# Optimization experiments

Measured on AMD Instinct MI355X. Metric: run time of the kernel, lower is better.

Reference implementation:

```python
import jax, jax.numpy as jnp
import numpy as np

DIM = 256
HEADS = 8
NX = NY = 48
RNG = 5
MAX_IDX = (RNG + 1) ** 2  # 36, padding token


def _make_tokens(nx, ny, rng):
    # Half-symmetric tokenization of 2D relative positions (Learnable_rel_pos_embedding.tokenize)
    xm, ym = np.meshgrid(np.arange(nx), np.arange(ny), indexing='ij')
    xm, ym = xm.ravel(), ym.ravel()
    dx = xm[None, :] - xm[:, None]
    dy = ym[None, :] - ym[:, None]
    tok = np.abs(dx) * (rng + 1) + np.abs(dy)
    tok[(np.abs(dx) > rng) | (np.abs(dy) > rng)] = MAX_IDX
    return tok.astype(np.int32)


def setup_inputs() -> dict:
    key = jax.random.key(0)
    ks = jax.random.split(key, 10)
    s = DIM ** -0.5
    x = jax.random.normal(ks[0], (1, DIM, NX, NY), dtype=jnp.float32)
    Wq = jax.random.normal(ks[1], (DIM, DIM), dtype=jnp.float32) * s
    bq = jax.random.normal(ks[2], (DIM,), dtype=jnp.float32) * 0.01
    Wk = jax.random.normal(ks[3], (DIM, DIM), dtype=jnp.float32) * s
    bk = jax.random.normal(ks[4], (DIM,), dtype=jnp.float32) * 0.01
    Wv = jax.random.normal(ks[5], (DIM, DIM), dtype=jnp.float32) * s
    bv = jax.random.normal(ks[6], (DIM,), dtype=jnp.float32) * 0.01
    Wp = jax.random.normal(ks[7], (DIM, DIM), dtype=jnp.float32) * s
    bp = jax.random.normal(ks[8], (DIM,), dtype=jnp.float32) * 0.01
    emb = jax.random.normal(ks[9], (MAX_IDX + 1, HEADS), dtype=jnp.float32) * 0.02
    tokens = jnp.asarray(_make_tokens(NX, NY, RNG))  # (N, N) int32
    return dict(x=x, Wq=Wq, bq=bq, Wk=Wk, bk=bk, Wv=Wv, bv=bv,
                Wp=Wp, bp=bp, emb=emb, tokens=tokens)


def reference(x, Wq, bq, Wk, bk, Wv, bv, Wp, bp, emb, tokens):
    B, C, nx, ny = x.shape
    H = emb.shape[1]
    hd = C // H
    N = nx * ny
    scale = hd ** -0.5

    def conv1x1(W, b, t):
        return (jnp.einsum('oc,bcxy->boxy', W, t) + b[None, :, None, None])

    # Q/K/V as 1x1 convs, split into heads: (B, H, hd, N)
    q = conv1x1(Wq, bq, x).reshape(B, H, hd, N)
    k = conv1x1(Wk, bk, x).reshape(B, H, hd, N)
    v = conv1x1(Wv, bv, x).reshape(B, H, hd, N)

    # attn_method=2: scores = scale*QK^T + relative positional bias
    scores = jnp.einsum('bhdn,bhdm->bhnm', q, k) * scale  # (B, H, N, N)

    # pos_type=5: embedding lookup over half-symmetric relative-position tokens
    pad = emb.shape[0] - 1
    emb_masked = emb.at[pad].set(0.0)  # padding_idx row is zero
    pe = emb_masked[tokens]            # (N, N, H)
    scores = scores + jnp.transpose(pe, (2, 0, 1))[None]

    attn = jax.nn.softmax(scores, axis=-1)
    out = jnp.einsum('bhnm,bhdm->bhdn', attn, v).reshape(B, C, nx, ny)
    out = conv1x1(Wp, bp, out)
    return out
```

## Files before the change

kernel.cpp:

```cpp
#include <hip/hip_runtime.h>

#define NN 2304
#define CC 256
#define HH 8
#define HD 32
#define NYY 48
#define SCALE 0.17677669529663687f

typedef __bf16 bf16_t;
typedef __bf16 bf8v __attribute__((ext_vector_type(8)));
typedef float f4v __attribute__((ext_vector_type(4)));

__device__ __forceinline__ f4v mfma16(bf8v a, bf8v b, f4v c) {
    return __builtin_amdgcn_mfma_f32_16x16x32_bf16(a, b, c, 0, 0, 0);
}

__global__ __launch_bounds__(256) void k_xT(const float* __restrict__ x,
                                            bf16_t* __restrict__ xT) {
    __shared__ float tile[64][33];
    const int c0 = (blockIdx.x & 7) * 32;
    const int n0 = (blockIdx.x >> 3) * 64;
    const int t = threadIdx.x;
    const int n = t & 63, cb = t >> 6;
#pragma unroll
    for (int cc = 0; cc < 8; cc++) {
        int c = cc * 4 + cb;
        tile[n][c] = x[(size_t)(c0 + c) * NN + n0 + n];
    }
    __syncthreads();
    const int c = t & 31, nb = t >> 5;
#pragma unroll
    for (int nn = 0; nn < 8; nn++) {
        int n2 = nn * 8 + nb;
        xT[(size_t)(n0 + n2) * CC + c0 + c] = (bf16_t)tile[n2][c];
    }
}

__global__ __launch_bounds__(256) void k_proj_qkv(
    const float* __restrict__ Wq, const float* __restrict__ bq,
    const float* __restrict__ Wk, const float* __restrict__ bk,
    const float* __restrict__ Wv, const float* __restrict__ bv,
    const bf16_t* __restrict__ xT,
    bf16_t* __restrict__ Qt, bf16_t* __restrict__ Kt, bf16_t* __restrict__ Vd) {
    const int mat = blockIdx.z;
    const float* W = (mat == 0) ? Wq : (mat == 1) ? Wk : Wv;
    const float* bias = (mat == 0) ? bq : (mat == 1) ? bk : bv;
    const int n0 = blockIdx.x * 64;
    const int o0 = blockIdx.y * 64;
    const int lane = threadIdx.x & 63;
    const int wave = threadIdx.x >> 6;
    const int l15 = lane & 15;
    const int quad = lane >> 4;
    const int orow = o0 + wave * 16;

    f4v acc[4];
#pragma unroll
    for (int i = 0; i < 4; i++) acc[i] = f4v{0.f, 0.f, 0.f, 0.f};

    for (int k0 = 0; k0 < CC; k0 += 32) {
        const float* wp = W + (size_t)(orow + l15) * CC + k0 + quad * 8;
        float4 wa = *(const float4*)wp;
        float4 wb = *(const float4*)(wp + 4);
        bf8v af;
        af[0] = (bf16_t)wa.x; af[1] = (bf16_t)wa.y;
        af[2] = (bf16_t)wa.z; af[3] = (bf16_t)wa.w;
        af[4] = (bf16_t)wb.x; af[5] = (bf16_t)wb.y;
        af[6] = (bf16_t)wb.z; af[7] = (bf16_t)wb.w;
#pragma unroll
        for (int nb = 0; nb < 4; nb++) {
            bf8v bfv = *(const bf8v*)(xT + (size_t)(n0 + nb * 16 + l15) * CC + k0 + quad * 8);
            acc[nb] = mfma16(af, bfv, acc[nb]);
        }
    }

#pragma unroll
    for (int r = 0; r < 4; r++) {
        const int o = orow + quad * 4 + r;
        const float bo = bias[o];
#pragma unroll
        for (int nb = 0; nb < 4; nb++) {
            const int n = n0 + nb * 16 + l15;
            float v = acc[nb][r] + bo;
            if (mat == 2) {
                Vd[(size_t)o * NN + n] = (bf16_t)v;
            } else {
                int h = o >> 5, d = o & 31;
                bf16_t* dst = (mat == 0) ? Qt : Kt;
                float vv = (mat == 0) ? v * SCALE : v;
                dst[(size_t)h * NN * HD + (size_t)n * HD + d] = (bf16_t)vv;
            }
        }
    }
}

__global__ __launch_bounds__(256) void k_attn(
    const bf16_t* __restrict__ Qt, const bf16_t* __restrict__ Kt,
    const bf16_t* __restrict__ Vd, const float* __restrict__ emb,
    bf16_t* __restrict__ Yt) {
    __shared__ float lds_emb[40];
    __shared__ bf16_t lds_p[4][16 * 32];
    const int h = blockIdx.x & 7;
    const int qt = blockIdx.x >> 3;
    const int t = threadIdx.x;
    if (t < 37) lds_emb[t] = (t < 36) ? emb[t * HH + h] : 0.0f;
    __syncthreads();

    const int wave = t >> 6, lane = t & 63;
    const int l15 = lane & 15, quad = lane >> 4;
    const int qg0 = qt * 64 + wave * 16;
    const bf16_t* Qh = Qt + (size_t)h * NN * HD;
    const bf16_t* Kh = Kt + (size_t)h * NN * HD;
    const bf16_t* Vh = Vd + (size_t)h * HD * NN;

    const bf8v aq = *(const bf8v*)(Qh + (size_t)(qg0 + l15) * HD + quad * 8);

    int xi[4], yi[4];
#pragma unroll
    for (int r = 0; r < 4; r++) {
        int qi = qg0 + quad * 4 + r;
        xi[r] = qi / NYY;
        yi[r] = qi - xi[r] * NYY;
    }

    f4v o0 = {0.f, 0.f, 0.f, 0.f}, o1 = {0.f, 0.f, 0.f, 0.f};
    const f4v z = {0.f, 0.f, 0.f, 0.f};
    float lsum[4] = {0.f, 0.f, 0.f, 0.f};
    bf16_t* pl = &lds_p[wave][0];

    for (int kb = 0; kb < NN; kb += 32) {
        bf8v kf0 = *(const bf8v*)(Kh + (size_t)(kb + l15) * HD + quad * 8);
        bf8v kf1 = *(const bf8v*)(Kh + (size_t)(kb + 16 + l15) * HD + quad * 8);
        bf8v vf0 = *(const bf8v*)(Vh + (size_t)l15 * NN + kb + quad * 8);
        bf8v vf1 = *(const bf8v*)(Vh + (size_t)(16 + l15) * NN + kb + quad * 8);
        f4v s0 = mfma16(aq, kf0, z);
        f4v s1 = mfma16(aq, kf1, z);
#pragma unroll
        for (int cb = 0; cb < 2; cb++) {
            const f4v& s = cb ? s1 : s0;
            int kj = kb + cb * 16 + l15;
            int xj = kj / NYY;
            int yj = kj - xj * NYY;
#pragma unroll
            for (int r = 0; r < 4; r++) {
                int dx = xi[r] - xj; dx = dx < 0 ? -dx : dx;
                int dy = yi[r] - yj; dy = dy < 0 ? -dy : dy;
                int tok = (dx > 5 || dy > 5) ? 36 : dx * 6 + dy;
                float p = __expf(s[r] + lds_emb[tok]);
                lsum[r] += p;
                pl[(quad * 4 + r) * 32 + cb * 16 + l15] = (bf16_t)p;
            }
        }
        bf8v ap = *(const bf8v*)(pl + l15 * 32 + quad * 8);
        o0 = mfma16(ap, vf0, o0);
        o1 = mfma16(ap, vf1, o1);
    }

#pragma unroll
    for (int r = 0; r < 4; r++) {
        float v = lsum[r];
#pragma unroll
        for (int m = 1; m < 16; m <<= 1) v += __shfl_xor(v, m, 64);
        float inv = 1.0f / v;
        int row = qg0 + quad * 4 + r;
        Yt[(size_t)row * CC + h * HD + l15] = (bf16_t)(o0[r] * inv);
        Yt[(size_t)row * CC + h * HD + 16 + l15] = (bf16_t)(o1[r] * inv);
    }
}

__global__ __launch_bounds__(256) void k_proj_out(
    const float* __restrict__ Wp, const float* __restrict__ bp,
    const bf16_t* __restrict__ Yt, float* __restrict__ out) {
    const int n0 = blockIdx.x * 64;
    const int o0 = blockIdx.y * 64;
    const int lane = threadIdx.x & 63;
    const int wave = threadIdx.x >> 6;
    const int l15 = lane & 15;
    const int quad = lane >> 4;
    const int orow = o0 + wave * 16;

    f4v acc[4];
#pragma unroll
    for (int i = 0; i < 4; i++) acc[i] = f4v{0.f, 0.f, 0.f, 0.f};

    for (int k0 = 0; k0 < CC; k0 += 32) {
        const float* wp = Wp + (size_t)(orow + l15) * CC + k0 + quad * 8;
        float4 wa = *(const float4*)wp;
        float4 wb = *(const float4*)(wp + 4);
        bf8v af;
        af[0] = (bf16_t)wa.x; af[1] = (bf16_t)wa.y;
        af[2] = (bf16_t)wa.z; af[3] = (bf16_t)wa.w;
        af[4] = (bf16_t)wb.x; af[5] = (bf16_t)wb.y;
        af[6] = (bf16_t)wb.z; af[7] = (bf16_t)wb.w;
#pragma unroll
        for (int nb = 0; nb < 4; nb++) {
            bf8v bv = *(const bf8v*)(Yt + (size_t)(n0 + nb * 16 + l15) * CC + k0 + quad * 8);
            acc[nb] = mfma16(af, bv, acc[nb]);
        }
    }

#pragma unroll
    for (int r = 0; r < 4; r++) {
        const int o = orow + quad * 4 + r;
        const float bo = bp[o];
#pragma unroll
        for (int nb = 0; nb < 4; nb++) {
            const int n = n0 + nb * 16 + l15;
            out[(size_t)o * NN + n] = acc[nb][r] + bo;
        }
    }
}

extern "C" void kernel_launch(void* const* d_in, const int* in_sizes, int n_in,
                              void* d_out, int out_size, void* d_ws, size_t ws_size,
                              hipStream_t stream) {
    const float* x   = (const float*)d_in[0];
    const float* Wq  = (const float*)d_in[1];
    const float* bq  = (const float*)d_in[2];
    const float* Wk  = (const float*)d_in[3];
    const float* bk  = (const float*)d_in[4];
    const float* Wv  = (const float*)d_in[5];
    const float* bv  = (const float*)d_in[6];
    const float* Wp  = (const float*)d_in[7];
    const float* bp  = (const float*)d_in[8];
    const float* emb = (const float*)d_in[9];
    float* out = (float*)d_out;

    bf16_t* xT = (bf16_t*)d_ws;
    bf16_t* Qt = xT + (size_t)NN * CC;
    bf16_t* Kt = Qt + (size_t)NN * CC;
    bf16_t* Vd = Kt + (size_t)NN * CC;
    bf16_t* Yt = Vd + (size_t)NN * CC;

    hipLaunchKernelGGL(k_xT, dim3(8 * 36), dim3(256), 0, stream, x, xT);
    hipLaunchKernelGGL(k_proj_qkv, dim3(36, 4, 3), dim3(256), 0, stream,
                       Wq, bq, Wk, bk, Wv, bv, xT, Qt, Kt, Vd);
    hipLaunchKernelGGL(k_attn, dim3(288), dim3(256), 0, stream, Qt, Kt, Vd, emb, Yt);
    hipLaunchKernelGGL(k_proj_out, dim3(36, 4), dim3(256), 0, stream, Wp, bp, Yt, out);
}
```

Before: 161.0 us.

## Split attention over key ranges, pre-convert weights to bf16, shrink projection tiles

Attention is split along the key dimension into up to 8 chunks per (query tile, head), raising the grid from 288 blocks to as many as 2304. Each chunk writes unnormalized fp32 partial outputs and row sums, which a new reduce kernel adds up and normalizes. Weights are converted to bf16 once in the prologue kernel, and the projection kernels use 32-column tiles to launch more blocks. The trade-off is extra workspace, another launch and global traffic for the partials. No running max is kept, and the earlier kernel did not keep one either.

```diff
diff --git a/kernel.cpp b/kernel.cpp
--- a/kernel.cpp
+++ b/kernel.cpp
@@ -15,37 +15,54 @@
     return __builtin_amdgcn_mfma_f32_16x16x32_bf16(a, b, c, 0, 0, 0);
 }
 
-__global__ __launch_bounds__(256) void k_xT(const float* __restrict__ x,
-                                            bf16_t* __restrict__ xT) {
-    __shared__ float tile[64][33];
-    const int c0 = (blockIdx.x & 7) * 32;
-    const int n0 = (blockIdx.x >> 3) * 64;
+__global__ __launch_bounds__(256) void k_pre(
+    const float* __restrict__ x, bf16_t* __restrict__ xT,
+    const float* __restrict__ Wq, const float* __restrict__ Wk,
+    const float* __restrict__ Wv, const float* __restrict__ Wp,
+    bf16_t* __restrict__ Wb) {
+    const int b = blockIdx.x;
     const int t = threadIdx.x;
-    const int n = t & 63, cb = t >> 6;
-#pragma unroll
-    for (int cc = 0; cc < 8; cc++) {
-        int c = cc * 4 + cb;
-        tile[n][c] = x[(size_t)(c0 + c) * NN + n0 + n];
-    }
-    __syncthreads();
-    const int c = t & 31, nb = t >> 5;
-#pragma unroll
-    for (int nn = 0; nn < 8; nn++) {
-        int n2 = nn * 8 + nb;
-        xT[(size_t)(n0 + n2) * CC + c0 + c] = (bf16_t)tile[n2][c];
+    if (b < 288) {
+        __shared__ float tile[64][33];
+        const int c0 = (b & 7) * 32;
+        const int n0 = (b >> 3) * 64;
+        const int n = t & 63, cb = t >> 6;
+#pragma unroll
+        for (int cc = 0; cc < 8; cc++) {
+            int c = cc * 4 + cb;
+            tile[n][c] = x[(size_t)(c0 + c) * NN + n0 + n];
+        }
+        __syncthreads();
+        const int c = t & 31, nb = t >> 5;
+#pragma unroll
+        for (int nn = 0; nn < 8; nn++) {
+            int n2 = nn * 8 + nb;
+            xT[(size_t)(n0 + n2) * CC + c0 + c] = (bf16_t)tile[n2][c];
+        }
+    } else {
+        const int wb = b - 288;
+        const int matid = wb >> 5;
+        const float* src = (matid == 0) ? Wq : (matid == 1) ? Wk : (matid == 2) ? Wv : Wp;
+        const int base = (wb & 31) * 2048 + t * 8;
+        float4 a = *(const float4*)(src + base);
+        float4 c = *(const float4*)(src + base + 4);
+        bf8v o;
+        o[0] = (bf16_t)a.x; o[1] = (bf16_t)a.y; o[2] = (bf16_t)a.z; o[3] = (bf16_t)a.w;
+        o[4] = (bf16_t)c.x; o[5] = (bf16_t)c.y; o[6] = (bf16_t)c.z; o[7] = (bf16_t)c.w;
+        *(bf8v*)(Wb + (size_t)matid * 65536 + base) = o;
     }
 }
 
 __global__ __launch_bounds__(256) void k_proj_qkv(
-    const float* __restrict__ Wq, const float* __restrict__ bq,
-    const float* __restrict__ Wk, const float* __restrict__ bk,
-    const float* __restrict__ Wv, const float* __restrict__ bv,
+    const bf16_t* __restrict__ Wb,
+    const float* __restrict__ bq, const float* __restrict__ bk,
+    const float* __restrict__ bv,
     const bf16_t* __restrict__ xT,
     bf16_t* __restrict__ Qt, bf16_t* __restrict__ Kt, bf16_t* __restrict__ Vd) {
     const int mat = blockIdx.z;
-    const float* W = (mat == 0) ? Wq : (mat == 1) ? Wk : Wv;
+    const bf16_t* W = Wb + (size_t)mat * 65536;
     const float* bias = (mat == 0) ? bq : (mat == 1) ? bk : bv;
-    const int n0 = blockIdx.x * 64;
+    const int n0 = blockIdx.x * 32;
     const int o0 = blockIdx.y * 64;
     const int lane = threadIdx.x & 63;
     const int wave = threadIdx.x >> 6;
@@ -53,24 +70,14 @@
     const int quad = lane >> 4;
     const int orow = o0 + wave * 16;
 
-    f4v acc[4];
-#pragma unroll
-    for (int i = 0; i < 4; i++) acc[i] = f4v{0.f, 0.f, 0.f, 0.f};
-
+    f4v acc0 = {0.f, 0.f, 0.f, 0.f}, acc1 = {0.f, 0.f, 0.f, 0.f};
+#pragma unroll
     for (int k0 = 0; k0 < CC; k0 += 32) {
-        const float* wp = W + (size_t)(orow + l15) * CC + k0 + quad * 8;
-        float4 wa = *(const float4*)wp;
-        float4 wb = *(const float4*)(wp + 4);
-        bf8v af;
-        af[0] = (bf16_t)wa.x; af[1] = (bf16_t)wa.y;
-        af[2] = (bf16_t)wa.z; af[3] = (bf16_t)wa.w;
-        af[4] = (bf16_t)wb.x; af[5] = (bf16_t)wb.y;
-        af[6] = (bf16_t)wb.z; af[7] = (bf16_t)wb.w;
-#pragma unroll
-        for (int nb = 0; nb < 4; nb++) {
-            bf8v bfv = *(const bf8v*)(xT + (size_t)(n0 + nb * 16 + l15) * CC + k0 + quad * 8);
-            acc[nb] = mfma16(af, bfv, acc[nb]);
-        }
+        bf8v af = *(const bf8v*)(W + (size_t)(orow + l15) * CC + k0 + quad * 8);
+        bf8v b0 = *(const bf8v*)(xT + (size_t)(n0 + l15) * CC + k0 + quad * 8);
+        bf8v b1 = *(const bf8v*)(xT + (size_t)(n0 + 16 + l15) * CC + k0 + quad * 8);
+        acc0 = mfma16(af, b0, acc0);
+        acc1 = mfma16(af, b1, acc1);
     }
 
 #pragma unroll
@@ -78,9 +85,9 @@
         const int o = orow + quad * 4 + r;
         const float bo = bias[o];
 #pragma unroll
-        for (int nb = 0; nb < 4; nb++) {
+        for (int nb = 0; nb < 2; nb++) {
             const int n = n0 + nb * 16 + l15;
-            float v = acc[nb][r] + bo;
+            float v = (nb ? acc1[r] : acc0[r]) + bo;
             if (mat == 2) {
                 Vd[(size_t)o * NN + n] = (bf16_t)v;
             } else {
@@ -93,14 +100,15 @@
     }
 }
 
-__global__ __launch_bounds__(256) void k_attn(
+__global__ __launch_bounds__(256) void k_attn_split(
     const bf16_t* __restrict__ Qt, const bf16_t* __restrict__ Kt,
     const bf16_t* __restrict__ Vd, const float* __restrict__ emb,
-    bf16_t* __restrict__ Yt) {
+    float* __restrict__ pO, float* __restrict__ pl, int L) {
     __shared__ float lds_emb[40];
     __shared__ bf16_t lds_p[4][16 * 32];
     const int h = blockIdx.x & 7;
     const int qt = blockIdx.x >> 3;
+    const int sidx = blockIdx.y;
     const int t = threadIdx.x;
     if (t < 37) lds_emb[t] = (t < 36) ? emb[t * HH + h] : 0.0f;
     __syncthreads();
@@ -125,9 +133,10 @@
     f4v o0 = {0.f, 0.f, 0.f, 0.f}, o1 = {0.f, 0.f, 0.f, 0.f};
     const f4v z = {0.f, 0.f, 0.f, 0.f};
     float lsum[4] = {0.f, 0.f, 0.f, 0.f};
-    bf16_t* pl = &lds_p[wave][0];
-
-    for (int kb = 0; kb < NN; kb += 32) {
+    bf16_t* plds = &lds_p[wave][0];
+
+    const int k_begin = sidx * L, k_end = k_begin + L;
+    for (int kb = k_begin; kb < k_end; kb += 32) {
         bf8v kf0 = *(const bf8v*)(Kh + (size_t)(kb + l15) * HD + quad * 8);
         bf8v kf1 = *(const bf8v*)(Kh + (size_t)(kb + 16 + l15) * HD + quad * 8);
         bf8v vf0 = *(const bf8v*)(Vh + (size_t)l15 * NN + kb + quad * 8);
@@ -147,30 +156,49 @@
                 int tok = (dx > 5 || dy > 5) ? 36 : dx * 6 + dy;
                 float p = __expf(s[r] + lds_emb[tok]);
                 lsum[r] += p;
-                pl[(quad * 4 + r) * 32 + cb * 16 + l15] = (bf16_t)p;
+                plds[(quad * 4 + r) * 32 + cb * 16 + l15] = (bf16_t)p;
             }
         }
-        bf8v ap = *(const bf8v*)(pl + l15 * 32 + quad * 8);
+        bf8v ap = *(const bf8v*)(plds + l15 * 32 + quad * 8);
         o0 = mfma16(ap, vf0, o0);
         o1 = mfma16(ap, vf1, o1);
     }
 
+    float* pO_s = pO + ((size_t)sidx * HH + h) * NN * HD;
+    float* pl_s = pl + ((size_t)sidx * HH + h) * NN;
 #pragma unroll
     for (int r = 0; r < 4; r++) {
         float v = lsum[r];
 #pragma unroll
         for (int m = 1; m < 16; m <<= 1) v += __shfl_xor(v, m, 64);
-        float inv = 1.0f / v;
         int row = qg0 + quad * 4 + r;
-        Yt[(size_t)row * CC + h * HD + l15] = (bf16_t)(o0[r] * inv);
-        Yt[(size_t)row * CC + h * HD + 16 + l15] = (bf16_t)(o1[r] * inv);
-    }
+        pO_s[(size_t)row * HD + l15] = o0[r];
+        pO_s[(size_t)row * HD + 16 + l15] = o1[r];
+        if (l15 == 0) pl_s[row] = v;
+    }
+}
+
+__global__ __launch_bounds__(256) void k_reduce(
+    const float* __restrict__ pO, const float* __restrict__ pl,
+    bf16_t* __restrict__ Yt, int S) {
+    const int e = blockIdx.x * 256 + threadIdx.x;
+    const int h = e / (NN * HD);
+    const int rem = e - h * (NN * HD);
+    const int q = rem >> 5;
+    const int d = rem & 31;
+    float so = 0.f, sl = 0.f;
+    for (int s = 0; s < S; s++) {
+        so += pO[((size_t)s * HH + h) * NN * HD + (size_t)q * HD + d];
+        sl += pl[((size_t)s * HH + h) * NN + q];
+    }
+    Yt[(size_t)q * CC + h * HD + d] = (bf16_t)(so / sl);
 }
 
 __global__ __launch_bounds__(256) void k_proj_out(
-    const float* __restrict__ Wp, const float* __restrict__ bp,
+    const bf16_t* __restrict__ Wb, const float* __restrict__ bp,
     const bf16_t* __restrict__ Yt, float* __restrict__ out) {
-    const int n0 = blockIdx.x * 64;
+    const bf16_t* W = Wb + (size_t)3 * 65536;
+    const int n0 = blockIdx.x * 32;
     const int o0 = blockIdx.y * 64;
     const int lane = threadIdx.x & 63;
     const int wave = threadIdx.x >> 6;
@@ -178,35 +206,22 @@
     const int quad = lane >> 4;
     const int orow = o0 + wave * 16;
 
-    f4v acc[4];
-#pragma unroll
-    for (int i = 0; i < 4; i++) acc[i] = f4v{0.f, 0.f, 0.f, 0.f};
-
+    f4v acc0 = {0.f, 0.f, 0.f, 0.f}, acc1 = {0.f, 0.f, 0.f, 0.f};
+#pragma unroll
     for (int k0 = 0; k0 < CC; k0 += 32) {
-        const float* wp = Wp + (size_t)(orow + l15) * CC + k0 + quad * 8;
-        float4 wa = *(const float4*)wp;
-        float4 wb = *(const float4*)(wp + 4);
-        bf8v af;
-        af[0] = (bf16_t)wa.x; af[1] = (bf16_t)wa.y;
-        af[2] = (bf16_t)wa.z; af[3] = (bf16_t)wa.w;
-        af[4] = (bf16_t)wb.x; af[5] = (bf16_t)wb.y;
-        af[6] = (bf16_t)wb.z; af[7] = (bf16_t)wb.w;
-#pragma unroll
-        for (int nb = 0; nb < 4; nb++) {
-            bf8v bv = *(const bf8v*)(Yt + (size_t)(n0 + nb * 16 + l15) * CC + k0 + quad * 8);
-            acc[nb] = mfma16(af, bv, acc[nb]);
-        }
+        bf8v af = *(const bf8v*)(W + (size_t)(orow + l15) * CC + k0 + quad * 8);
+        bf8v b0 = *(const bf8v*)(Yt + (size_t)(n0 + l15) * CC + k0 + quad * 8);
+        bf8v b1 = *(const bf8v*)(Yt + (size_t)(n0 + 16 + l15) * CC + k0 + quad * 8);
+        acc0 = mfma16(af, b0, acc0);
+        acc1 = mfma16(af, b1, acc1);
     }
 
 #pragma unroll
     for (int r = 0; r < 4; r++) {
         const int o = orow + quad * 4 + r;
         const float bo = bp[o];
-#pragma unroll
-        for (int nb = 0; nb < 4; nb++) {
-            const int n = n0 + nb * 16 + l15;
-            out[(size_t)o * NN + n] = acc[nb][r] + bo;
-        }
+        out[(size_t)o * NN + n0 + l15] = acc0[r] + bo;
+        out[(size_t)o * NN + n0 + 16 + l15] = acc1[r] + bo;
     }
 }
 
@@ -230,10 +245,25 @@
     bf16_t* Kt = Qt + (size_t)NN * CC;
     bf16_t* Vd = Kt + (size_t)NN * CC;
     bf16_t* Yt = Vd + (size_t)NN * CC;
-
-    hipLaunchKernelGGL(k_xT, dim3(8 * 36), dim3(256), 0, stream, x, xT);
-    hipLaunchKernelGGL(k_proj_qkv, dim3(36, 4, 3), dim3(256), 0, stream,
-                       Wq, bq, Wk, bk, Wv, bv, xT, Qt, Kt, Vd);
-    hipLaunchKernelGGL(k_attn, dim3(288), dim3(256), 0, stream, Qt, Kt, Vd, emb, Yt);
-    hipLaunchKernelGGL(k_proj_out, dim3(36, 4), dim3(256), 0, stream, Wp, bp, Yt, out);
-}
+    bf16_t* Wb = Yt + (size_t)NN * CC;
+    float*  pO = (float*)(Wb + (size_t)4 * CC * CC);
+
+    const size_t base_bytes = (size_t)5 * NN * CC * 2 + (size_t)4 * CC * CC * 2;
+    const size_t per_split = (size_t)HH * NN * HD * 4 + (size_t)HH * NN * 4;
+    int S = 1;
+    if (base_bytes + 8 * per_split <= ws_size) S = 8;
+    else if (base_bytes + 4 * per_split <= ws_size) S = 4;
+    else if (base_bytes + 2 * per_split <= ws_size) S = 2;
+    float* pl = pO + (size_t)S * HH * NN * HD;
+    const int L = NN / S;
+
+    hipLaunchKernelGGL(k_pre, dim3(288 + 128), dim3(256), 0, stream,
+                       x, xT, Wq, Wk, Wv, Wp, Wb);
+    hipLaunchKernelGGL(k_proj_qkv, dim3(72, 4, 3), dim3(256), 0, stream,
+                       Wb, bq, bk, bv, xT, Qt, Kt, Vd);
+    hipLaunchKernelGGL(k_attn_split, dim3(288, S), dim3(256), 0, stream,
+                       Qt, Kt, Vd, emb, pO, pl, L);
+    hipLaunchKernelGGL(k_reduce, dim3((HH * NN * HD) / 256), dim3(256), 0, stream,
+                       pO, pl, Yt, S);
+    hipLaunchKernelGGL(k_proj_out, dim3(72, 4), dim3(256), 0, stream, Wb, bp, Yt, out);
+}
```

Result: faster. 151.1 us (-6.2%).
